# Kernel tuning notes

Measured on AMD Instinct MI355X. Metric: run time of the kernel, lower is better.

Reference implementation:

```python
import jax, jax.numpy as jnp
import numpy as np

B, S, HID = 2, 2048, 1024
NH, HD = 4, 256
SCALE = HD ** -0.5


def _rope(x, fr, fi):
    # x: [B,S,NH,HD]; fr/fi: [S,HD//2]
    b, s, n, d = x.shape
    xr = x.reshape(b, s, n, d // 2, 2)
    re, im = xr[..., 0], xr[..., 1]
    fr = fr[None, :, None, :]
    fi = fi[None, :, None, :]
    rr = re * fr - im * fi
    ri = re * fi + im * fr
    return jnp.stack((rr, ri), axis=-1).reshape(b, s, n, d)


def setup_inputs() -> dict:
    key = jax.random.key(0)
    k1, k2, k3 = jax.random.split(key, 3)
    hidden_states = jax.random.normal(k1, (B, S, HID), dtype=jnp.float32)
    # RoPE frequencies (standard theta=10000)
    inv_freq = 1.0 / (10000.0 ** (np.arange(0, HD, 2, dtype=np.float32) / HD))  # [HD//2]
    t = np.arange(S, dtype=np.float32)
    ang = np.outer(t, inv_freq)  # [S, HD//2]
    freqs_real = jnp.asarray(np.cos(ang), dtype=jnp.float32)
    freqs_imag = jnp.asarray(np.sin(ang), dtype=jnp.float32)
    # causal additive mask [1,1,S,S]
    causal = jnp.tril(jnp.ones((S, S), dtype=bool))
    mask = jnp.where(causal, 0.0, -1e9).astype(jnp.float32)[None, None]
    W_qkv = jax.random.normal(k2, (3 * HID, HID), dtype=jnp.float32) * (HID ** -0.5)
    W_o = jax.random.normal(k3, (HID, HID), dtype=jnp.float32) * (HID ** -0.5)
    return {"hidden_states": hidden_states, "freqs_real": freqs_real,
            "freqs_imag": freqs_imag, "mask": mask, "W_qkv": W_qkv, "W_o": W_o}


def reference(hidden_states, freqs_real, freqs_imag, mask, W_qkv, W_o):
    b, s, _ = hidden_states.shape
    qkv = hidden_states @ W_qkv.T  # [B,S,3*HID]
    qkv = qkv.reshape(b, s, 3, NH, HD)
    q, k, v = qkv[:, :, 0], qkv[:, :, 1], qkv[:, :, 2]
    q = _rope(q, freqs_real, freqs_imag)
    k = _rope(k, freqs_real, freqs_imag)
    scores = jnp.einsum('bqhd,bkhd->bhqk', q * SCALE, k) + mask  # [B,NH,S,S]
    probs = jax.nn.softmax(scores, axis=-1)
    attn = jnp.einsum('bhqk,bkhd->bqhd', probs, v).reshape(b, s, HID)
    return attn @ W_o.T
```

## Files before the change

### kernel.cpp

```cpp
#include <hip/hip_runtime.h>
#include <stdint.h>

#define NB 2
#define NS 2048
#define NHID 1024
#define NHEADS 4
#define DHEAD 256
#define NP 128
#define QK_SCALE 0.0625f

typedef unsigned short ushort_t;
typedef __bf16 bf16x8 __attribute__((ext_vector_type(8)));
typedef float floatx4 __attribute__((ext_vector_type(4)));
typedef short shortx8 __attribute__((ext_vector_type(8)));
typedef unsigned short ushortx4 __attribute__((ext_vector_type(4)));
typedef unsigned short ushortx8 __attribute__((ext_vector_type(8)));

__device__ __forceinline__ float bf2f(ushort_t u) {
    unsigned int x = ((unsigned int)u) << 16;
    return __builtin_bit_cast(float, x);
}
__device__ __forceinline__ ushort_t f2bf(float f) {
    unsigned int u = __builtin_bit_cast(unsigned int, f);
    u += 0x7fff + ((u >> 16) & 1);
    return (ushort_t)(u >> 16);
}

__device__ __forceinline__ floatx4 mfma16(bf16x8 a, bf16x8 b, floatx4 c) {
    return __builtin_amdgcn_mfma_f32_16x16x32_bf16(a, b, c, 0, 0, 0);
}

__device__ __forceinline__ void gload_lds16(const void* g, void* l) {
    __builtin_amdgcn_global_load_lds(
        (const __attribute__((address_space(1))) void*)g,
        (__attribute__((address_space(3))) void*)l, 16, 0, 0);
}

#define N4_H (4096 * 1024 / 4)
#define N4_WQ (3072 * 1024 / 4)
#define N4_WO (1024 * 1024 / 4)
__global__ __launch_bounds__(256) void cast3_kernel(const float* __restrict__ inH,
                                                    const float* __restrict__ inWq,
                                                    const float* __restrict__ inWo,
                                                    ushort_t* __restrict__ out) {
    int i = blockIdx.x * 256 + threadIdx.x;
    const float* src;
    int j = i;
    if (i < N4_H) {
        src = inH;
    } else if (i < N4_H + N4_WQ) {
        src = inWq; j = i - N4_H;
    } else {
        src = inWo; j = i - (N4_H + N4_WQ);
    }
    float4 v = ((const float4*)src)[j];
    ushortx4 o = { f2bf(v.x), f2bf(v.y), f2bf(v.z), f2bf(v.w) };
    ((ushortx4*)out)[i] = o;
}


__global__ __launch_bounds__(256) void gemm_bt_f32s(const ushort_t* __restrict__ A,
                                                    const ushort_t* __restrict__ Bt,
                                                    float* __restrict__ C0,
                                                    float* __restrict__ C1,
                                                    int M, int N, int K) {
    __shared__ ushort_t sA[128 * 64];
    __shared__ ushort_t sB[128 * 64];
    const int t = threadIdx.x;
    const int f = blockIdx.x;
    const int xcd = f & 7;
    const int idx = f >> 3;
    const int im = idx >> 4;
    const int in = (idx >> 1) & 7;
    const int kz = idx & 1;
    const int m0 = (xcd * 4 + im) * 128;
    const int n0 = in * 128;
    float* Cout = kz ? C1 : C0;
    const int kbeg = kz * (K / 2), kend = kbeg + K / 2;
    const int w = t >> 6, l = t & 63;
    const int wm = (w >> 1) * 64, wn = (w & 1) * 64;
    const int lc = l & 15, lq = l >> 4;

    floatx4 acc[4][4];
#pragma unroll
    for (int i = 0; i < 4; i++)
#pragma unroll
        for (int j = 0; j < 4; j++) acc[i][j] = (floatx4){0.f, 0.f, 0.f, 0.f};

    const int srow = w * 8 + (l >> 3);
    const int scol = ((((l & 7) - (l >> 3)) & 7)) * 8;
    const ushort_t* Ag = A + (size_t)(m0 + srow) * K + scol;
    const ushort_t* Bg = Bt + (size_t)(n0 + srow) * K + scol;
    ushort_t* lA = &sA[(size_t)t * 8];
    ushort_t* lB = &sB[(size_t)t * 8];

    for (int kk = kbeg; kk < kend; kk += 64) {
        __syncthreads();
#pragma unroll
        for (int j = 0; j < 4; j++) {
            gload_lds16(Ag + kk + (size_t)j * 32 * K, lA + j * 2048);
            gload_lds16(Bg + kk + (size_t)j * 32 * K, lB + j * 2048);
        }
        __syncthreads();
#pragma unroll
        for (int ks = 0; ks < 2; ks++) {
            bf16x8 af[4], bfv[4];
#pragma unroll
            for (int i = 0; i < 4; i++) {
                int R = wm + i * 16 + lc;
                af[i] = *(const bf16x8*)&sA[R * 64 + ((ks * 4 + lq + R) & 7) * 8];
            }
#pragma unroll
            for (int j = 0; j < 4; j++) {
                int R = wn + j * 16 + lc;
                bfv[j] = *(const bf16x8*)&sB[R * 64 + ((ks * 4 + lq + R) & 7) * 8];
            }
#pragma unroll
            for (int i = 0; i < 4; i++)
#pragma unroll
                for (int j = 0; j < 4; j++)
                    acc[i][j] = mfma16(af[i], bfv[j], acc[i][j]);
        }
    }

#pragma unroll
    for (int i = 0; i < 4; i++) {
        int row = m0 + wm + i * 16 + lq * 4;
#pragma unroll
        for (int j = 0; j < 4; j++) {
            int col = n0 + wn + j * 16 + lc;
#pragma unroll
            for (int r = 0; r < 4; r++)
                Cout[(size_t)(row + r) * N + col] = acc[i][j][r];
        }
    }
}

__global__ __launch_bounds__(256) void add_f32(const float* __restrict__ a,
                                               const float* __restrict__ b,
                                               float* __restrict__ o, int n4) {
    int i = blockIdx.x * 256 + threadIdx.x;
    if (i < n4) {
        float4 x = ((const float4*)a)[i];
        float4 y = ((const float4*)b)[i];
        float4 z = { x.x + y.x, x.y + y.y, x.z + y.z, x.w + y.w };
        ((float4*)o)[i] = z;
    }
}

__global__ __launch_bounds__(256) void gemm_qkv(const ushort_t* __restrict__ A,
                                                const ushort_t* __restrict__ Bt,
                                                const float* __restrict__ fre,
                                                const float* __restrict__ fim,
                                                ushort_t* __restrict__ Q,
                                                ushort_t* __restrict__ Kk,
                                                ushort_t* __restrict__ Vt) {
    const int M_K = 1024;
    __shared__ ushort_t sA0[128 * 64];
    __shared__ ushort_t sA1[128 * 64];
    __shared__ ushort_t sB0[128 * 64];
    __shared__ ushort_t sB1[128 * 64];
    const int t = threadIdx.x;
    const int f = blockIdx.x;
    const int xcd = f & 7;
    const int idx = f >> 3;
    const int mr = xcd & 3, nr = xcd >> 2;
    const int im = idx & 7, in = idx >> 3;
    const int m0 = (mr * 8 + im) * 128;
    const int n0 = (nr * 12 + in) * 128;
    const int w = t >> 6, l = t & 63;
    const int wm = (w >> 1) * 64, wn = (w & 1) * 64;
    const int lc = l & 15, lq = l >> 4;

    floatx4 acc[4][4];
#pragma unroll
    for (int i = 0; i < 4; i++)
#pragma unroll
        for (int j = 0; j < 4; j++) acc[i][j] = (floatx4){0.f, 0.f, 0.f, 0.f};

    const int srow = w * 8 + (l >> 3);
    const int scol = ((((l & 7) - (l >> 3)) & 7)) * 8;
    const ushort_t* Ag = A + (size_t)(m0 + srow) * M_K + scol;
    const ushort_t* Bg = Bt + (size_t)(n0 + srow) * M_K + scol;
    const int lofs = t * 8;

    auto stage = [&](ushort_t* lA, ushort_t* lB, int kk) {
#pragma unroll
        for (int j = 0; j < 4; j++) {
            gload_lds16(Ag + kk + (size_t)j * 32 * M_K, lA + j * 2048);
            gload_lds16(Bg + kk + (size_t)j * 32 * M_K, lB + j * 2048);
        }
    };
    auto compute = [&](const ushort_t* cA, const ushort_t* cB) {
#pragma unroll
        for (int ks = 0; ks < 2; ks++) {
            bf16x8 af[4], bfv[4];
#pragma unroll
            for (int i = 0; i < 4; i++) {
                int R = wm + i * 16 + lc;
                af[i] = *(const bf16x8*)&cA[R * 64 + ((ks * 4 + lq + R) & 7) * 8];
            }
#pragma unroll
            for (int j = 0; j < 4; j++) {
                int R = wn + j * 16 + lc;
                bfv[j] = *(const bf16x8*)&cB[R * 64 + ((ks * 4 + lq + R) & 7) * 8];
            }
#pragma unroll
            for (int i = 0; i < 4; i++)
#pragma unroll
                for (int j = 0; j < 4; j++)
                    acc[i][j] = mfma16(af[i], bfv[j], acc[i][j]);
        }
    };

    stage(&sA0[lofs], &sB0[lofs], 0);
    asm volatile("s_waitcnt vmcnt(0)" ::: "memory");
    __builtin_amdgcn_s_barrier();

#pragma unroll 1
    for (int s = 0; s < 16; s += 2) {
        if (s + 1 < 16) stage(&sA1[lofs], &sB1[lofs], (s + 1) * 64);
        compute(sA0, sB0);
        asm volatile("s_waitcnt vmcnt(0)" ::: "memory");
        __builtin_amdgcn_s_barrier();
        if (s + 2 < 16) stage(&sA0[lofs], &sB0[lofs], (s + 2) * 64);
        compute(sA1, sB1);
        asm volatile("s_waitcnt vmcnt(0)" ::: "memory");
        __builtin_amdgcn_s_barrier();
    }

    const int sect = n0 >> 10;
#pragma unroll
    for (int i = 0; i < 4; i++) {
        int row = m0 + wm + i * 16 + lq * 4;
        int b = row >> 11;
        int srow2 = row & 2047;
#pragma unroll
        for (int j = 0; j < 4; j++) {
            int col = n0 + wn + j * 16 + lc;
            int d = col & 255;
            int h = (col >> 8) & 3;
            int bh = b * NHEADS + h;
            if (sect == 2) {
                ushortx4 pack = { f2bf(acc[i][j][0]), f2bf(acc[i][j][1]),
                                  f2bf(acc[i][j][2]), f2bf(acc[i][j][3]) };
                *(ushortx4*)&Vt[((size_t)bh * 256 + d) * NS + srow2] = pack;
            } else {
                int p = d >> 1;
                int odd = d & 1;
                ushort_t* dst = (sect == 0) ? Q : Kk;
#pragma unroll
                for (int r = 0; r < 4; r++) {
                    float v = acc[i][j][r];
                    float vp = __shfl_xor(v, 1);
                    int s = srow2 + r;
                    float c = fre[s * NP + p], si = fim[s * NP + p];
                    float out = odd ? (vp * si + v * c) : (v * c - vp * si);
                    if (sect == 0) out *= QK_SCALE;
                    dst[((size_t)bh * NS + s) * DHEAD + d] = f2bf(out);
                }
            }
        }
    }
}

#define BQ3 128
#define BKV3 64
#define PPAD 72
#define CHCAP 6
#define NPART_BH 51
#define OPART_SPLIT 224

__global__ __launch_bounds__(256, 2) void flash_attn4(const ushort_t* __restrict__ Q,
                                                      const ushort_t* __restrict__ K,
                                                      const ushort_t* __restrict__ Vt,
                                                      ushort_t* __restrict__ OpA,
                                                      ushort_t* __restrict__ OpB,
                                                      float* __restrict__ ml) {
    __shared__ ushort_t sK[BKV3 * 256];
    __shared__ ushort_t sV[DHEAD * 64];
    __shared__ ushort_t sP[4][16 * PPAD];

    int rem = blockIdx.x, qt = 15, nsp;
    for (;;) {
        nsp = (2 * (qt + 1) + CHCAP - 1) / CHCAP;
        if (rem < nsp) break;
        rem -= nsp;
        qt--;
    }
    const int nch = 2 * (qt + 1);
    const int cbeg = rem * CHCAP;
    const int cend = (cbeg + CHCAP < nch) ? cbeg + CHCAP : nch;

    const int h = blockIdx.y, b = blockIdx.z;
    const int t = threadIdx.x, w = t >> 6, l = t & 63;
    const int lc = l & 15, lq = l >> 4;
    const int bh = b * NHEADS + h;
    const size_t base = (size_t)bh * NS * DHEAD;
    const int q0 = qt * BQ3;

    const int krb = w * 2 + (l >> 5);
    const int kck = ((l & 31) - (krb & 7)) & 31;
    const size_t koff = (size_t)krb * 256 + kck * 8;
    const int vrb = w * 8 + (l >> 3);
    const int vck = ((l & 7) - (vrb & 7)) & 7;
    const size_t voff = (size_t)vrb * NS + vck * 8;
    ushort_t* dK = &sK[w * 512 + l * 8];
    ushort_t* dV = &sV[w * 512 + l * 8];

    bf16x8 qf[2][8];
#pragma unroll
    for (int gq = 0; gq < 2; gq++) {
        const ushort_t* qrow = Q + base + (size_t)(q0 + w * 32 + gq * 16 + lc) * DHEAD + lq * 8;
#pragma unroll
        for (int dk = 0; dk < 8; dk++) qf[gq][dk] = *(const bf16x8*)(qrow + dk * 32);
    }

    floatx4 accO[2][16];
#pragma unroll
    for (int gq = 0; gq < 2; gq++)
#pragma unroll
        for (int j = 0; j < 16; j++) accO[gq][j] = (floatx4){0.f, 0.f, 0.f, 0.f};
    float lrun[2][4] = {{0.f, 0.f, 0.f, 0.f}, {0.f, 0.f, 0.f, 0.f}};

    for (int kc = cbeg; kc < cend; kc++) {
        const int kb = kc * BKV3;
        __syncthreads();
        {
            const ushort_t* ksrc = K + base + (size_t)kb * 256 + koff;
            const ushort_t* vsrc = Vt + base + kb + voff;
#pragma unroll
            for (int j = 0; j < 8; j++)
                gload_lds16(ksrc + j * (8 * 256), dK + j * 2048);
#pragma unroll
            for (int j = 0; j < 8; j++)
                gload_lds16(vsrc + j * (32 * NS), dV + j * 2048);
        }
        __syncthreads();

        floatx4 sfr[2][4];
#pragma unroll
        for (int gq = 0; gq < 2; gq++)
#pragma unroll
            for (int g = 0; g < 4; g++) sfr[gq][g] = (floatx4){0.f, 0.f, 0.f, 0.f};
#pragma unroll
        for (int dk = 0; dk < 8; dk++) {
#pragma unroll
            for (int g = 0; g < 4; g++) {
                int R = g * 16 + lc;
                int phys = (dk * 4 + lq + (R & 7)) & 31;
                bf16x8 bk = *(const bf16x8*)&sK[R * 256 + phys * 8];
                sfr[0][g] = mfma16(qf[0][dk], bk, sfr[0][g]);
                sfr[1][g] = mfma16(qf[1][dk], bk, sfr[1][g]);
            }
        }

        if (kc >= nch - 2) {
#pragma unroll
            for (int gq = 0; gq < 2; gq++)
#pragma unroll
                for (int g = 0; g < 4; g++) {
                    int kg = kb + g * 16 + lc;
                    int qr = q0 + w * 32 + gq * 16 + lq * 4;
#pragma unroll
                    for (int r = 0; r < 4; r++)
                        if (kg > qr + r) sfr[gq][g][r] = -1e30f;
                }
        }

        ushort_t* pw = sP[w];
#pragma unroll
        for (int gq = 0; gq < 2; gq++) {
#pragma unroll
            for (int g = 0; g < 4; g++)
#pragma unroll
                for (int r = 0; r < 4; r++) {
                    float p = __expf(sfr[gq][g][r]);
                    lrun[gq][r] += p;
                    pw[(lq * 4 + r) * PPAD + g * 16 + lc] = f2bf(p);
                }
            bf16x8 ap0 = *(const bf16x8*)&pw[lc * PPAD + lq * 8];
            bf16x8 ap1 = *(const bf16x8*)&pw[lc * PPAD + 32 + lq * 8];
#pragma unroll
            for (int j = 0; j < 16; j++) {
                int D = j * 16 + lc;
                int ph0 = (lq + (D & 7)) & 7;
                int ph1 = (4 + lq + (D & 7)) & 7;
                bf16x8 bv0 = *(const bf16x8*)&sV[D * 64 + ph0 * 8];
                bf16x8 bv1 = *(const bf16x8*)&sV[D * 64 + ph1 * 8];
                accO[gq][j] = mfma16(ap0, bv0, accO[gq][j]);
                accO[gq][j] = mfma16(ap1, bv1, accO[gq][j]);
            }
        }
    }

    const int pid = bh * NPART_BH + blockIdx.x;
    ushort_t* op = (pid < OPART_SPLIT) ? OpA + (size_t)pid * (128 * 256)
                                       : OpB + (size_t)(pid - OPART_SPLIT) * (128 * 256);
#pragma unroll
    for (int gq = 0; gq < 2; gq++) {
#pragma unroll
        for (int r = 0; r < 4; r++) {
            int row = w * 32 + gq * 16 + lq * 4 + r;
#pragma unroll
            for (int j = 0; j < 16; j++)
                op[row * 256 + j * 16 + lc] = f2bf(accO[gq][j][r]);
            float lv = lrun[gq][r];
#pragma unroll
            for (int off = 1; off < 16; off <<= 1) lv += __shfl_xor(lv, off);
            if (lc == 0) ml[(size_t)pid * 128 + row] = lv;
        }
    }
}

__global__ __launch_bounds__(256) void combine_parts2(const ushort_t* __restrict__ OpA,
                                                      const ushort_t* __restrict__ OpB,
                                                      const float* __restrict__ ml,
                                                      ushort_t* __restrict__ O) {
    const int qt = blockIdx.x >> 3, rsub = blockIdx.x & 7;
    const int h = blockIdx.y, b = blockIdx.z;
    const int bh = b * NHEADS + h;
    int bbase = 0;
    for (int q = 15; q > qt; q--) bbase += (2 * (q + 1) + CHCAP - 1) / CHCAP;
    const int nsp = (2 * (qt + 1) + CHCAP - 1) / CHCAP;
    const int pid0 = bh * NPART_BH + bbase;

    const int t = threadIdx.x;
    const int rl = t >> 4;
    const int c0 = (t & 15) * 16;
    const int row = rsub * 16 + rl;

    float so[16];
#pragma unroll
    for (int k = 0; k < 16; k++) so[k] = 0.f;
    float sl = 0.f;

    for (int i = 0; i < nsp; i++) {
        int pid = pid0 + i;
        const ushort_t* op = (pid < OPART_SPLIT)
                                 ? OpA + (size_t)pid * (128 * 256)
                                 : OpB + (size_t)(pid - OPART_SPLIT) * (128 * 256);
        const ushort_t* p = op + row * 256 + c0;
        ushortx8 a0 = *(const ushortx8*)p;
        ushortx8 a1 = *(const ushortx8*)(p + 8);
#pragma unroll
        for (int k = 0; k < 8; k++) {
            so[k] += bf2f(a0[k]);
            so[8 + k] += bf2f(a1[k]);
        }
        sl += ml[(size_t)pid * 128 + row];
    }

    float inv = 1.f / sl;
    ushortx8 o0, o1;
#pragma unroll
    for (int k = 0; k < 8; k++) {
        o0[k] = f2bf(so[k] * inv);
        o1[k] = f2bf(so[8 + k] * inv);
    }
    int s = qt * BQ3 + row;
    ushort_t* dst = O + ((size_t)(b * NS + s) * NHEADS + h) * DHEAD + c0;
    *(ushortx8*)dst = o0;
    *(ushortx8*)(dst + 8) = o1;
}

extern "C" void kernel_launch(void* const* d_in, const int* in_sizes, int n_in,
                              void* d_out, int out_size, void* d_ws, size_t ws_size,
                              hipStream_t stream) {
    const float* hidden = (const float*)d_in[0];
    const float* fre = (const float*)d_in[1];
    const float* fim = (const float*)d_in[2];
    const float* Wqkv = (const float*)d_in[4];
    const float* Wo = (const float*)d_in[5];

    char* ws = (char*)d_ws;
    ushort_t* hb    = (ushort_t*)(ws);
    ushort_t* wqkvb = (ushort_t*)(ws + 8388608);
    ushort_t* wob   = (ushort_t*)(ws + 14680064);
    ushort_t* qb    = (ushort_t*)(ws + 16777216);
    ushort_t* kb    = (ushort_t*)(ws + 25165824);
    ushort_t* vtb   = (ushort_t*)(ws + 33554432);
    ushort_t* OpA   = (ushort_t*)(ws);
    ushort_t* OpB   = (ushort_t*)(ws + 41943040);
    ushort_t* oattn = (ushort_t*)(ws + 16777216);
    float*    gP0   = (float*)(ws + 25165824);
    float*    gP1   = (float*)(ws + 41943040);
    float*    ml    = (float*)(ws + 58720256);

    cast3_kernel<<<(N4_H + N4_WQ + N4_WO) / 256, 256, 0, stream>>>(hidden, Wqkv, Wo, hb);

    gemm_qkv<<<dim3(768), 256, 0, stream>>>(
        hb, wqkvb, fre, fim, qb, kb, vtb);

    flash_attn4<<<dim3(NPART_BH, NHEADS, NB), 256, 0, stream>>>(qb, kb, vtb, OpA, OpB, ml);
    combine_parts2<<<dim3(128, NHEADS, NB), 256, 0, stream>>>(OpA, OpB, ml, oattn);

    gemm_bt_f32s<<<dim3(512), 256, 0, stream>>>(
        oattn, wob, gP0, gP1, 4096, 1024, 1024);
    add_f32<<<4096, 256, 0, stream>>>(gP0, gP1, (float*)d_out, 4096 * 1024 / 4);
}
```

Before: 212.2 us.

## Use 4-stage K=32 LDS pipeline in output and QKV GEMMs

Both GEMM kernels switch from 64-wide K tiles (single-buffered in the split-K output GEMM, double-buffered in the QKV GEMM) to four rotating 32-wide K buffers. Loads for three stages are kept in flight and waited on with partial vmcnt counts, with one barrier per stage. The aim is to hide global-to-LDS latency behind MFMA work and drop the extra synchronisation. The cost is more barriers per unit of K, smaller MFMA batches per barrier, and a new LDS swizzle for the narrower rows.

```diff
diff --git a/kernel.cpp b/kernel.cpp
--- a/kernel.cpp
+++ b/kernel.cpp
@@ -64,8 +64,8 @@
                                                     float* __restrict__ C0,
                                                     float* __restrict__ C1,
                                                     int M, int N, int K) {
-    __shared__ ushort_t sA[128 * 64];
-    __shared__ ushort_t sB[128 * 64];
+    __shared__ ushort_t sA[4][128 * 32];
+    __shared__ ushort_t sB[4][128 * 32];
     const int t = threadIdx.x;
     const int f = blockIdx.x;
     const int xcd = f & 7;
@@ -76,7 +76,7 @@
     const int m0 = (xcd * 4 + im) * 128;
     const int n0 = in * 128;
     float* Cout = kz ? C1 : C0;
-    const int kbeg = kz * (K / 2), kend = kbeg + K / 2;
+    const int kbeg = kz * (K / 2);
     const int w = t >> 6, l = t & 63;
     const int wm = (w >> 1) * 64, wn = (w & 1) * 64;
     const int lc = l & 15, lq = l >> 4;
@@ -87,41 +87,62 @@
 #pragma unroll
         for (int j = 0; j < 4; j++) acc[i][j] = (floatx4){0.f, 0.f, 0.f, 0.f};
 
-    const int srow = w * 8 + (l >> 3);
-    const int scol = ((((l & 7) - (l >> 3)) & 7)) * 8;
-    const ushort_t* Ag = A + (size_t)(m0 + srow) * K + scol;
-    const ushort_t* Bg = Bt + (size_t)(n0 + srow) * K + scol;
-    ushort_t* lA = &sA[(size_t)t * 8];
-    ushort_t* lB = &sB[(size_t)t * 8];
-
-    for (int kk = kbeg; kk < kend; kk += 64) {
-        __syncthreads();
+    const int srow = w * 16 + (l >> 2);
+    const int scol = (((l & 3) - (l >> 2)) & 3) * 8;
+    const ushort_t* Ag = A + (size_t)(m0 + srow) * K + scol + kbeg;
+    const ushort_t* Bg = Bt + (size_t)(n0 + srow) * K + scol + kbeg;
+    const int lofs = t * 8;
+
+    auto stage = [&](int bsel, int kk) {
+        ushort_t* lA = &sA[bsel][lofs];
+        ushort_t* lB = &sB[bsel][lofs];
+        gload_lds16(Ag + kk, lA);
+        gload_lds16(Ag + kk + (size_t)64 * K, lA + 2048);
+        gload_lds16(Bg + kk, lB);
+        gload_lds16(Bg + kk + (size_t)64 * K, lB + 2048);
+    };
+    auto compute = [&](int bsel) {
+        const ushort_t* cA = sA[bsel];
+        const ushort_t* cB = sB[bsel];
+        bf16x8 af[4], bfv[4];
+#pragma unroll
+        for (int i = 0; i < 4; i++) {
+            int R = wm + i * 16 + lc;
+            af[i] = *(const bf16x8*)&cA[R * 32 + ((lq + R) & 3) * 8];
+        }
 #pragma unroll
         for (int j = 0; j < 4; j++) {
-            gload_lds16(Ag + kk + (size_t)j * 32 * K, lA + j * 2048);
-            gload_lds16(Bg + kk + (size_t)j * 32 * K, lB + j * 2048);
-        }
-        __syncthreads();
-#pragma unroll
-        for (int ks = 0; ks < 2; ks++) {
-            bf16x8 af[4], bfv[4];
-#pragma unroll
-            for (int i = 0; i < 4; i++) {
-                int R = wm + i * 16 + lc;
-                af[i] = *(const bf16x8*)&sA[R * 64 + ((ks * 4 + lq + R) & 7) * 8];
-            }
-#pragma unroll
-            for (int j = 0; j < 4; j++) {
-                int R = wn + j * 16 + lc;
-                bfv[j] = *(const bf16x8*)&sB[R * 64 + ((ks * 4 + lq + R) & 7) * 8];
-            }
-#pragma unroll
-            for (int i = 0; i < 4; i++)
-#pragma unroll
-                for (int j = 0; j < 4; j++)
-                    acc[i][j] = mfma16(af[i], bfv[j], acc[i][j]);
-        }
-    }
+            int R = wn + j * 16 + lc;
+            bfv[j] = *(const bf16x8*)&cB[R * 32 + ((lq + R) & 3) * 8];
+        }
+#pragma unroll
+        for (int i = 0; i < 4; i++)
+#pragma unroll
+            for (int j = 0; j < 4; j++)
+                acc[i][j] = mfma16(af[i], bfv[j], acc[i][j]);
+    };
+
+    stage(0, 0); stage(1, 32); stage(2, 64);
+#pragma unroll 1
+    for (int s = 0; s <= 16 - 4; ++s) {
+        asm volatile("s_waitcnt vmcnt(8)" ::: "memory");
+        __builtin_amdgcn_sched_barrier(0);
+        __builtin_amdgcn_s_barrier();
+        compute(s & 3);
+        stage((s + 3) & 3, (s + 3) * 32);
+    }
+    asm volatile("s_waitcnt vmcnt(8)" ::: "memory");
+    __builtin_amdgcn_sched_barrier(0);
+    __builtin_amdgcn_s_barrier();
+    compute(13 & 3);
+    asm volatile("s_waitcnt vmcnt(4)" ::: "memory");
+    __builtin_amdgcn_sched_barrier(0);
+    __builtin_amdgcn_s_barrier();
+    compute(14 & 3);
+    asm volatile("s_waitcnt vmcnt(0)" ::: "memory");
+    __builtin_amdgcn_sched_barrier(0);
+    __builtin_amdgcn_s_barrier();
+    compute(15 & 3);
 
 #pragma unroll
     for (int i = 0; i < 4; i++) {
@@ -156,10 +177,8 @@
                                                 ushort_t* __restrict__ Kk,
                                                 ushort_t* __restrict__ Vt) {
     const int M_K = 1024;
-    __shared__ ushort_t sA0[128 * 64];
-    __shared__ ushort_t sA1[128 * 64];
-    __shared__ ushort_t sB0[128 * 64];
-    __shared__ ushort_t sB1[128 * 64];
+    __shared__ ushort_t sA[4][128 * 32];
+    __shared__ ushort_t sB[4][128 * 32];
     const int t = threadIdx.x;
     const int f = blockIdx.x;
     const int xcd = f & 7;
@@ -178,56 +197,62 @@
 #pragma unroll
         for (int j = 0; j < 4; j++) acc[i][j] = (floatx4){0.f, 0.f, 0.f, 0.f};
 
-    const int srow = w * 8 + (l >> 3);
-    const int scol = ((((l & 7) - (l >> 3)) & 7)) * 8;
+    const int srow = w * 16 + (l >> 2);
+    const int scol = (((l & 3) - (l >> 2)) & 3) * 8;
     const ushort_t* Ag = A + (size_t)(m0 + srow) * M_K + scol;
     const ushort_t* Bg = Bt + (size_t)(n0 + srow) * M_K + scol;
     const int lofs = t * 8;
 
-    auto stage = [&](ushort_t* lA, ushort_t* lB, int kk) {
+    auto stage = [&](int bsel, int kk) {
+        ushort_t* lA = &sA[bsel][lofs];
+        ushort_t* lB = &sB[bsel][lofs];
+        gload_lds16(Ag + kk, lA);
+        gload_lds16(Ag + kk + (size_t)64 * M_K, lA + 2048);
+        gload_lds16(Bg + kk, lB);
+        gload_lds16(Bg + kk + (size_t)64 * M_K, lB + 2048);
+    };
+    auto compute = [&](int bsel) {
+        const ushort_t* cA = sA[bsel];
+        const ushort_t* cB = sB[bsel];
+        bf16x8 af[4], bfv[4];
+#pragma unroll
+        for (int i = 0; i < 4; i++) {
+            int R = wm + i * 16 + lc;
+            af[i] = *(const bf16x8*)&cA[R * 32 + ((lq + R) & 3) * 8];
+        }
 #pragma unroll
         for (int j = 0; j < 4; j++) {
-            gload_lds16(Ag + kk + (size_t)j * 32 * M_K, lA + j * 2048);
-            gload_lds16(Bg + kk + (size_t)j * 32 * M_K, lB + j * 2048);
-        }
+            int R = wn + j * 16 + lc;
+            bfv[j] = *(const bf16x8*)&cB[R * 32 + ((lq + R) & 3) * 8];
+        }
+#pragma unroll
+        for (int i = 0; i < 4; i++)
+#pragma unroll
+            for (int j = 0; j < 4; j++)
+                acc[i][j] = mfma16(af[i], bfv[j], acc[i][j]);
     };
-    auto compute = [&](const ushort_t* cA, const ushort_t* cB) {
-#pragma unroll
-        for (int ks = 0; ks < 2; ks++) {
-            bf16x8 af[4], bfv[4];
-#pragma unroll
-            for (int i = 0; i < 4; i++) {
-                int R = wm + i * 16 + lc;
-                af[i] = *(const bf16x8*)&cA[R * 64 + ((ks * 4 + lq + R) & 7) * 8];
-            }
-#pragma unroll
-            for (int j = 0; j < 4; j++) {
-                int R = wn + j * 16 + lc;
-                bfv[j] = *(const bf16x8*)&cB[R * 64 + ((ks * 4 + lq + R) & 7) * 8];
-            }
-#pragma unroll
-            for (int i = 0; i < 4; i++)
-#pragma unroll
-                for (int j = 0; j < 4; j++)
-                    acc[i][j] = mfma16(af[i], bfv[j], acc[i][j]);
-        }
-    };
-
-    stage(&sA0[lofs], &sB0[lofs], 0);
+
+    stage(0, 0); stage(1, 32); stage(2, 64);
+#pragma unroll 1
+    for (int s = 0; s <= 32 - 4; ++s) {
+        asm volatile("s_waitcnt vmcnt(8)" ::: "memory");
+        __builtin_amdgcn_sched_barrier(0);
+        __builtin_amdgcn_s_barrier();
+        compute(s & 3);
+        stage((s + 3) & 3, (s + 3) * 32);
+    }
+    asm volatile("s_waitcnt vmcnt(8)" ::: "memory");
+    __builtin_amdgcn_sched_barrier(0);
+    __builtin_amdgcn_s_barrier();
+    compute(29 & 3);
+    asm volatile("s_waitcnt vmcnt(4)" ::: "memory");
+    __builtin_amdgcn_sched_barrier(0);
+    __builtin_amdgcn_s_barrier();
+    compute(30 & 3);
     asm volatile("s_waitcnt vmcnt(0)" ::: "memory");
+    __builtin_amdgcn_sched_barrier(0);
     __builtin_amdgcn_s_barrier();
-
-#pragma unroll 1
-    for (int s = 0; s < 16; s += 2) {
-        if (s + 1 < 16) stage(&sA1[lofs], &sB1[lofs], (s + 1) * 64);
-        compute(sA0, sB0);
-        asm volatile("s_waitcnt vmcnt(0)" ::: "memory");
-        __builtin_amdgcn_s_barrier();
-        if (s + 2 < 16) stage(&sA0[lofs], &sB0[lofs], (s + 2) * 64);
-        compute(sA1, sB1);
-        asm volatile("s_waitcnt vmcnt(0)" ::: "memory");
-        __builtin_amdgcn_s_barrier();
-    }
+    compute(31 & 3);
 
     const int sect = n0 >> 10;
 #pragma unroll
```

Result: no change. 209.2 us (-1.4%).
